# Optimization experiments

Hardware: AMD Instinct MI355X
Metric: run time of the kernel (lower is better)

## Reference

```python
import jax, jax.numpy as jnp
import numpy as np

B, H, W, S = 4, 512, 512, 40
DZ = 0.1            # slice thickness
FOCUS_SLICE = 25    # back-propagation slice count
Z_PLANE = 2.0       # focus plane offset
PAD = 32            # output crop


def setup_inputs() -> dict:
    key = jax.random.key(0)
    ks = jax.random.split(key, 8)
    sample_re = jax.random.normal(ks[0], (B, H, W, S), jnp.float32) * 0.01
    sample_im = jax.random.normal(ks[1], (B, H, W, S), jnp.float32) * 0.01
    planewave_re = jax.random.normal(ks[2], (B, H, W), jnp.float32)
    planewave_im = jax.random.normal(ks[3], (B, H, W), jnp.float32)
    # kz strictly positive so 1/(2*kz) is finite (mask + nan-fix kept for faithfulness)
    kz = jax.random.uniform(ks[4], (H, W), jnp.float32) + 0.5
    otf_abs = jax.random.uniform(ks[5], (H, W), jnp.float32)
    green_mask = (jax.random.uniform(ks[6], (H, W), jnp.float32) < 0.7).astype(jnp.float32)
    otf_phase = jax.random.normal(ks[7], (H, W), jnp.float32) * 0.1
    return dict(sample_re=sample_re, sample_im=sample_im,
                planewave_re=planewave_re, planewave_im=planewave_im,
                kz=kz, otf_abs=otf_abs, green_mask=green_mask, otf_phase=otf_phase)


def reference(sample_re, sample_im, planewave_re, planewave_im, kz, otf_abs, green_mask, otf_phase):
    sample = (sample_re + 1j * sample_im).astype(jnp.complex64)        # [B,H,W,S]
    planewave = (planewave_re + 1j * planewave_im).astype(jnp.complex64)  # [B,H,W]
    kzc = kz.astype(jnp.complex64)

    # module constants: prop_kernel = exp(prop_kernel_pha * dz), prop_kernel_pha = 1j*kz
    prop_kernel = jnp.exp(1j * kzc * DZ)                               # [H,W]
    green = (1j * prop_kernel / (2.0 * kzc)) * green_mask.astype(jnp.complex64)
    green = jnp.where(jnp.isnan(green), jnp.zeros((), green.dtype), green)

    # _propegate_to_last_slice_Multi_Born (oblique_factor=None)
    inc0 = jnp.fft.fft2(planewave)                                     # fft over last two dims
    sample_s = jnp.moveaxis(sample, -1, 0)                             # [S,B,H,W]

    def step(inc, slab):
        u = inc * prop_kernel
        scat = green * jnp.fft.fft2(jnp.fft.ifft2(inc) * slab * DZ)
        return u + scat, None

    inc, _ = jax.lax.scan(step, inc0, sample_s)

    # _propegate_to_center_focus_slice
    pk_center = jnp.conj(prop_kernel ** FOCUS_SLICE)
    pk_focus = prop_kernel ** (Z_PLANE / DZ)
    inc = inc * pk_center * pk_focus

    # _pupil_constrain_abs_square_output with OTF_input provided
    otf_update = (otf_abs * jnp.exp(1j * otf_phase)).astype(jnp.complex64)
    out = jnp.fft.ifft2(inc * otf_update[None])
    return jnp.abs(out)[:, PAD:-PAD, PAD:-PAD]                          # [B, H-2*PAD, W-2*PAD]
```

## Files before the change

### kernel.cpp

```cpp
#include <hip/hip_runtime.h>
#include <math.h>

#define HW_ (512 * 512)

__device__ inline float2 cadd(float2 a, float2 b){ return make_float2(a.x+b.x, a.y+b.y); }
__device__ inline float2 csub(float2 a, float2 b){ return make_float2(a.x-b.x, a.y-b.y); }
__device__ inline float2 cmulf(float2 a, float2 b){ return make_float2(a.x*b.x-a.y*b.y, a.x*b.y+a.y*b.x); }
__device__ inline float bf2f(unsigned short u){ return __uint_as_float(((unsigned int)u) << 16); }
__device__ inline unsigned short f2bf(float f){
    unsigned int x = __float_as_uint(f);
    x += 0x7fffu + ((x >> 16) & 1u);
    return (unsigned short)(x >> 16);
}

template<bool INV>
__device__ inline void dft8(const float2 a[8], float2 X[8]) {
    const float C = 0.70710678118654752440f;
    float2 t0 = cadd(a[0], a[4]), t4 = csub(a[0], a[4]);
    float2 t1 = cadd(a[1], a[5]), d1 = csub(a[1], a[5]);
    float2 t2 = cadd(a[2], a[6]), d2 = csub(a[2], a[6]);
    float2 t3 = cadd(a[3], a[7]), d3 = csub(a[3], a[7]);
    float2 t5, t6, t7;
    if (!INV) {
        t5 = make_float2(C*(d1.x + d1.y), C*(d1.y - d1.x));
        t6 = make_float2(d2.y, -d2.x);
        t7 = make_float2(C*(d3.y - d3.x), -C*(d3.x + d3.y));
    } else {
        t5 = make_float2(C*(d1.x - d1.y), C*(d1.y + d1.x));
        t6 = make_float2(-d2.y, d2.x);
        t7 = make_float2(-C*(d3.x + d3.y), C*(d3.x - d3.y));
    }
    float2 u0 = cadd(t0, t2), u2 = csub(t0, t2);
    float2 u1 = cadd(t1, t3), e3 = csub(t1, t3);
    float2 u3 = INV ? make_float2(-e3.y, e3.x) : make_float2(e3.y, -e3.x);
    float2 u4 = cadd(t4, t6), u6 = csub(t4, t6);
    float2 u5 = cadd(t5, t7), e7 = csub(t5, t7);
    float2 u7 = INV ? make_float2(-e7.y, e7.x) : make_float2(e7.y, -e7.x);
    X[0] = cadd(u0, u1); X[4] = csub(u0, u1);
    X[2] = cadd(u2, u3); X[6] = csub(u2, u3);
    X[1] = cadd(u4, u5); X[5] = csub(u4, u5);
    X[3] = cadd(u6, u7); X[7] = csub(u6, u7);
}

template<bool INV>
__device__ inline void fft512_reg(float2 a[8], float2* __restrict__ xch,
                                  int lane, float2 T1, float2 T2)
{
    float2 tw1 = INV ? make_float2(T1.x, -T1.y) : T1;
    float2 tw2 = INV ? make_float2(T2.x, -T2.y) : T2;
    const int rdo = lane + (lane >> 3);
    float2 b[8];

    dft8<INV>(a, b);
    { float2 w = tw1;
      #pragma unroll
      for (int k = 1; k < 8; ++k) { b[k] = cmulf(b[k], w); w = cmulf(w, tw1); } }
    #pragma unroll
    for (int k = 0; k < 8; ++k) xch[9*lane + k] = b[k];
    __asm__ volatile("s_waitcnt lgkmcnt(0)" ::: "memory");
    #pragma unroll
    for (int j = 0; j < 8; ++j) a[j] = xch[rdo + 72*j];

    dft8<INV>(a, b);
    { float2 w = tw2;
      #pragma unroll
      for (int k = 1; k < 8; ++k) { b[k] = cmulf(b[k], w); w = cmulf(w, tw2); } }
    { const int wbase = (lane & 7) + 72 * (lane >> 3);
      #pragma unroll
      for (int k = 0; k < 8; ++k) xch[wbase + 9*k] = b[k]; }
    __asm__ volatile("s_waitcnt lgkmcnt(0)" ::: "memory");
    #pragma unroll
    for (int j = 0; j < 8; ++j) b[j] = xch[rdo + 72*j];

    dft8<INV>(b, a);
}

__global__ __launch_bounds__(256)
void k_pre(const float* __restrict__ kz, const float* __restrict__ otfa,
           const float* __restrict__ gmask, const float* __restrict__ otfp,
           float2* __restrict__ propT, float2* __restrict__ greenT,
           float2* __restrict__ MT)
{
    __shared__ float2 tp[32*33], tg[32*33], tm[32*33];
    const int tid = threadIdx.x;
    const int w0 = (blockIdx.x & 15) << 5;
    const int h0 = (blockIdx.x >> 4) << 5;
    const int ww = tid & 31, hh = tid >> 5;
    #pragma unroll
    for (int p = 0; p < 4; ++p) {
        int h = hh + p*8;
        int idx = (h0 + h)*512 + w0 + ww;
        float k = kz[idx];
        float sn, cs; __sincosf(k * 0.1f, &sn, &cs);
        float inv2 = 0.5f / k * gmask[idx];
        float phase = otfp[idx] - k * 0.5f;
        float s2, c2; __sincosf(phase, &s2, &c2);
        float oa = otfa[idx];
        tp[h*33 + ww] = make_float2(cs, sn);
        tg[h*33 + ww] = make_float2(-sn*inv2, cs*inv2);
        tm[h*33 + ww] = make_float2(oa*c2, oa*s2);
    }
    __syncthreads();
    #pragma unroll
    for (int p = 0; p < 4; ++p) {
        int wrow = hh + p*8;
        size_t o = (size_t)(w0 + wrow)*512 + h0 + ww;
        propT[o]  = tp[ww*33 + wrow];
        greenT[o] = tg[ww*33 + wrow];
        MT[o]     = tm[ww*33 + wrow];
    }
}

__global__ __launch_bounds__(256)
void k_transpose(const float* __restrict__ sre, const float* __restrict__ sim,
                 ushort2* __restrict__ sampT)
{
    __shared__ ushort2 tile[40 * 129];
    const int bh = blockIdx.x;
    const int b = bh >> 9, h = bh & 511;
    const size_t src_base = (size_t)bh * (512 * 40);
    const float2* sre2 = (const float2*)(sre + src_base);
    const float2* sim2 = (const float2*)(sim + src_base);
    for (int chunk = 0; chunk < 4; ++chunk) {
        const int w0 = chunk * 128;
        const int base2 = w0 * 20;
        __syncthreads();
        for (int j = threadIdx.x; j < 128 * 20; j += 256) {
            float2 re = sre2[base2 + j];
            float2 im = sim2[base2 + j];
            int w = j / 20;
            int s = (j - w * 20) * 2;
            tile[s*129 + w]       = make_ushort2(f2bf(re.x), f2bf(im.x));
            tile[(s+1)*129 + w]   = make_ushort2(f2bf(re.y), f2bf(im.y));
        }
        __syncthreads();
        for (int j = threadIdx.x; j < 40 * 64; j += 256) {
            int s = j >> 6, w2 = (j & 63) << 1;
            ushort2 u0 = tile[s*129 + w2], u1 = tile[s*129 + w2 + 1];
            *(ushort4*)&sampT[(((size_t)s*4 + b)*512 + h)*512 + w0 + w2] =
                make_ushort4(u0.x, u0.y, u1.x, u1.y);
        }
    }
}

__global__ __launch_bounds__(256)
void k_row(float2* __restrict__ fld,
           const float* __restrict__ pwre, const float* __restrict__ pwim,
           const ushort2* __restrict__ sampT,
           float* __restrict__ finout,
           int mode, int slice)
{
    __shared__ float2 xchall[4 * 576];
    const int tid = threadIdx.x, lane = tid & 63, wv = tid >> 6;
    float2* xch = &xchall[wv * 576];
    float s1, c1, s2, c2;
    __sincosf(-6.2831853071795864769f * (float)lane / 512.0f, &s1, &c1);
    __sincosf(-6.2831853071795864769f * (float)(lane >> 3) / 64.0f, &s2, &c2);
    const float2 T1 = make_float2(c1, s1), T2 = make_float2(c2, s2);

    const int r = blockIdx.x * 4 + wv;
    int b, h;
    if (mode == 2) { b = r / 448; h = 32 + (r - b * 448); }
    else           { b = r >> 9;  h = r & 511; }
    const size_t rbase = ((size_t)b * 512 + h) * 512;
    float2 a[8];

    if (mode == 0) {
        #pragma unroll
        for (int j = 0; j < 8; ++j) {
            int w = lane + (j << 6);
            a[j] = make_float2(pwre[rbase + w], pwim[rbase + w]);
        }
        fft512_reg<false>(a, xch, lane, T1, T2);
        #pragma unroll
        for (int j = 0; j < 8; ++j) fld[rbase + lane + (j << 6)] = a[j];
        return;
    }

    #pragma unroll
    for (int j = 0; j < 8; ++j) a[j] = fld[rbase + lane + (j << 6)];
    fft512_reg<true>(a, xch, lane, T1, T2);

    if (mode == 2) {
        float* orow = finout + ((size_t)b * 448 + (h - 32)) * 448;
        #pragma unroll
        for (int j = 0; j < 8; ++j) {
            int w = lane + (j << 6);
            if (w >= 32 && w < 480) {
                float2 v = a[j];
                orow[w - 32] = sqrtf(v.x*v.x + v.y*v.y) * (1.0f / 512.0f);
            }
        }
        return;
    }

    const float scale = 0.1f / 512.0f;
    const size_t sbase = (((size_t)slice * 4 + b) * 512 + h) * 512;
    #pragma unroll
    for (int j = 0; j < 8; ++j) {
        int w = lane + (j << 6);
        ushort2 u = sampT[sbase + w];
        float sr = bf2f(u.x), si = bf2f(u.y);
        float2 v = a[j];
        a[j] = make_float2((v.x*sr - v.y*si) * scale, (v.x*si + v.y*sr) * scale);
    }
    fft512_reg<false>(a, xch, lane, T1, T2);
    #pragma unroll
    for (int j = 0; j < 8; ++j) fld[rbase + lane + (j << 6)] = a[j];
}

__global__ __launch_bounds__(512)
void k_col(float2* __restrict__ fld,
           float2* __restrict__ incT,
           const float2* __restrict__ propT, const float2* __restrict__ greenT,
           const float2* __restrict__ MT, int mode)
{
    __shared__ float2 tile[512 * 9];
    const int tid = threadIdx.x;
    const int lane = tid & 63, wv = tid >> 6;
    const int b = blockIdx.x >> 6;
    const int w0 = (blockIdx.x & 63) << 3;
    const int c = tid & 7, hb = tid >> 3;
    const size_t gbase = (size_t)b * HW_ + w0;

    float s1, c1, s2, c2;
    __sincosf(-6.2831853071795864769f * (float)lane / 512.0f, &s1, &c1);
    __sincosf(-6.2831853071795864769f * (float)(lane >> 3) / 64.0f, &s2, &c2);
    const float2 T1 = make_float2(c1, s1), T2 = make_float2(c2, s2);

    #pragma unroll
    for (int j = 0; j < 8; ++j) {
        int h = hb + (j << 6);
        tile[h*9 + c] = fld[gbase + (size_t)h * 512 + c];
    }
    __syncthreads();
    float2 a[8];
    const int w = w0 + wv;
    #pragma unroll
    for (int j = 0; j < 8; ++j) a[j] = tile[(lane + (j << 6)) * 9 + wv];
    __syncthreads();
    float2* xch = &tile[wv * 576];

    fft512_reg<false>(a, xch, lane, T1, T2);

    const size_t ibase = ((size_t)b * 512 + w) * 512;
    const size_t pbase = (size_t)w * 512;
    if (mode == 0) {
        #pragma unroll
        for (int k = 0; k < 8; ++k) incT[ibase + lane + (k << 6)] = a[k];
        return;
    }
    #pragma unroll
    for (int k = 0; k < 8; ++k) {
        int h = lane + (k << 6);
        float2 p  = propT[pbase + h];
        float2 g  = greenT[pbase + h];
        float2 io = incT[ibase + h];
        float2 nw = make_float2(p.x*io.x - p.y*io.y + g.x*a[k].x - g.y*a[k].y,
                                p.x*io.y + p.y*io.x + g.x*a[k].y + g.y*a[k].x);
        if (mode == 2) nw = cmulf(nw, MT[pbase + h]);
        else           incT[ibase + h] = nw;
        a[k] = nw;
    }

    fft512_reg<true>(a, xch, lane, T1, T2);
    __syncthreads();
    const float inv = 1.0f / 512.0f;
    #pragma unroll
    for (int k = 0; k < 8; ++k)
        tile[(lane + (k << 6)) * 9 + wv] = make_float2(a[k].x * inv, a[k].y * inv);
    __syncthreads();
    #pragma unroll
    for (int j = 0; j < 8; ++j) {
        int h = hb + (j << 6);
        fld[gbase + (size_t)h * 512 + c] = tile[h*9 + c];
    }
}

extern "C" void kernel_launch(void* const* d_in, const int* in_sizes, int n_in,
                              void* d_out, int out_size, void* d_ws, size_t ws_size,
                              hipStream_t stream)
{
    (void)in_sizes; (void)n_in; (void)out_size; (void)ws_size;
    const float* sre   = (const float*)d_in[0];
    const float* simg  = (const float*)d_in[1];
    const float* pwre  = (const float*)d_in[2];
    const float* pwim  = (const float*)d_in[3];
    const float* kz    = (const float*)d_in[4];
    const float* otfa  = (const float*)d_in[5];
    const float* gmask = (const float*)d_in[6];
    const float* otfp  = (const float*)d_in[7];

    char* ws = (char*)d_ws;
    size_t off = 0;
    float2* propT  = (float2*)(ws + off); off += (size_t)HW_ * 8;
    float2* greenT = (float2*)(ws + off); off += (size_t)HW_ * 8;
    float2* MT     = (float2*)(ws + off); off += (size_t)HW_ * 8;
    float2* incT   = (float2*)(ws + off); off += (size_t)4 * HW_ * 8;
    float2* fld    = (float2*)(ws + off); off += (size_t)4 * HW_ * 8;
    ushort2* sampT = (ushort2*)(ws + off);

    k_pre<<<256, 256, 0, stream>>>(kz, otfa, gmask, otfp, propT, greenT, MT);
    k_transpose<<<2048, 256, 0, stream>>>(sre, simg, sampT);

    k_row<<<512, 256, 0, stream>>>(fld, pwre, pwim, nullptr, nullptr, 0, 0);
    k_col<<<256, 512, 0, stream>>>(fld, incT, propT, greenT, MT, 0);

    for (int s = 0; s < 40; ++s) {
        k_row<<<512, 256, 0, stream>>>(fld, nullptr, nullptr, sampT, nullptr, 1, s);
        k_col<<<256, 512, 0, stream>>>(fld, incT, propT, greenT, MT, (s == 39) ? 2 : 1);
    }
    k_row<<<448, 256, 0, stream>>>(fld, nullptr, nullptr, nullptr, (float*)d_out, 2, 0);
}
```

Before: 1.359 ms.

## Drop incT buffer by keeping field row-FFT form and storing scattered field in fp16

Rather than keeping the spectrum incT in a separate transposed buffer, k_col now redoes the column FFT of the row-transformed field fldA each step. The scattered term goes through a new fp16 buffer written by k_row, so incT is never read or written. The transpose kernel is also rebuilt to use four times more blocks, float4 loads and an XOR-swizzled shared tile with 16-byte stores. This cuts global traffic per slice and the 8 MB incT stream, but it adds a second column FFT per step and fp16 rounding error on the scattered field.

```diff
diff --git a/kernel.cpp b/kernel.cpp
--- a/kernel.cpp
+++ b/kernel.cpp
@@ -1,4 +1,5 @@
 #include <hip/hip_runtime.h>
+#include <hip/hip_fp16.h>
 #include <math.h>
 
 #define HW_ (512 * 512)
@@ -115,36 +116,40 @@
 void k_transpose(const float* __restrict__ sre, const float* __restrict__ sim,
                  ushort2* __restrict__ sampT)
 {
-    __shared__ ushort2 tile[40 * 129];
-    const int bh = blockIdx.x;
+    __shared__ __align__(16) ushort2 tile[40 * 128];
+    const int bh = blockIdx.x >> 2;
+    const int chunk = blockIdx.x & 3;
     const int b = bh >> 9, h = bh & 511;
-    const size_t src_base = (size_t)bh * (512 * 40);
-    const float2* sre2 = (const float2*)(sre + src_base);
-    const float2* sim2 = (const float2*)(sim + src_base);
-    for (int chunk = 0; chunk < 4; ++chunk) {
-        const int w0 = chunk * 128;
-        const int base2 = w0 * 20;
-        __syncthreads();
-        for (int j = threadIdx.x; j < 128 * 20; j += 256) {
-            float2 re = sre2[base2 + j];
-            float2 im = sim2[base2 + j];
-            int w = j / 20;
-            int s = (j - w * 20) * 2;
-            tile[s*129 + w]       = make_ushort2(f2bf(re.x), f2bf(im.x));
-            tile[(s+1)*129 + w]   = make_ushort2(f2bf(re.y), f2bf(im.y));
-        }
-        __syncthreads();
-        for (int j = threadIdx.x; j < 40 * 64; j += 256) {
-            int s = j >> 6, w2 = (j & 63) << 1;
-            ushort2 u0 = tile[s*129 + w2], u1 = tile[s*129 + w2 + 1];
-            *(ushort4*)&sampT[(((size_t)s*4 + b)*512 + h)*512 + w0 + w2] =
-                make_ushort4(u0.x, u0.y, u1.x, u1.y);
-        }
+    const int w0 = chunk << 7;
+    const float4* sre4 = (const float4*)(sre + (size_t)bh * 20480) + chunk * 1280;
+    const float4* sim4 = (const float4*)(sim + (size_t)bh * 20480) + chunk * 1280;
+    #pragma unroll
+    for (int i = 0; i < 5; ++i) {
+        int j = threadIdx.x + (i << 8);
+        float4 re = sre4[j];
+        float4 im = sim4[j];
+        int w = j / 10;
+        int m = j - w * 10;
+        ushort2* row = &tile[(m << 2) * 128 + (w ^ ((m & 7) << 2))];
+        row[0]   = make_ushort2(f2bf(re.x), f2bf(im.x));
+        row[128] = make_ushort2(f2bf(re.y), f2bf(im.y));
+        row[256] = make_ushort2(f2bf(re.z), f2bf(im.z));
+        row[384] = make_ushort2(f2bf(re.w), f2bf(im.w));
+    }
+    __syncthreads();
+    #pragma unroll
+    for (int i = 0; i < 5; ++i) {
+        int j = threadIdx.x + (i << 8);
+        int s = j >> 5, q = j & 31;
+        int qp = q ^ ((s >> 2) & 7);
+        uint4 v = *(const uint4*)&tile[(s << 7) + (qp << 2)];
+        *(uint4*)&sampT[(((size_t)s * 4 + b) * 512 + h) * 512 + w0 + (q << 2)] = v;
     }
 }
 
 __global__ __launch_bounds__(256)
-void k_row(float2* __restrict__ fld,
+void k_row(float2* __restrict__ fldA,
+           ushort2* __restrict__ fld2,
            const float* __restrict__ pwre, const float* __restrict__ pwim,
            const ushort2* __restrict__ sampT,
            float* __restrict__ finout,
@@ -173,12 +178,12 @@
         }
         fft512_reg<false>(a, xch, lane, T1, T2);
         #pragma unroll
-        for (int j = 0; j < 8; ++j) fld[rbase + lane + (j << 6)] = a[j];
+        for (int j = 0; j < 8; ++j) fldA[rbase + lane + (j << 6)] = a[j];
         return;
     }
 
     #pragma unroll
-    for (int j = 0; j < 8; ++j) a[j] = fld[rbase + lane + (j << 6)];
+    for (int j = 0; j < 8; ++j) a[j] = fldA[rbase + lane + (j << 6)];
     fft512_reg<true>(a, xch, lane, T1, T2);
 
     if (mode == 2) {
@@ -206,16 +211,22 @@
     }
     fft512_reg<false>(a, xch, lane, T1, T2);
     #pragma unroll
-    for (int j = 0; j < 8; ++j) fld[rbase + lane + (j << 6)] = a[j];
+    for (int j = 0; j < 8; ++j) {
+        float2 v = a[j];
+        fld2[rbase + lane + (j << 6)] =
+            make_ushort2(__half_as_ushort(__float2half(v.x)),
+                         __half_as_ushort(__float2half(v.y)));
+    }
 }
 
 __global__ __launch_bounds__(512)
-void k_col(float2* __restrict__ fld,
-           float2* __restrict__ incT,
+void k_col(float2* __restrict__ fldA,
+           const ushort2* __restrict__ fld2,
            const float2* __restrict__ propT, const float2* __restrict__ greenT,
-           const float2* __restrict__ MT, int mode)
-{
-    __shared__ float2 tile[512 * 9];
+           const float2* __restrict__ MT, int last)
+{
+    __shared__ float2 tileA[512 * 9];
+    __shared__ ushort2 tile2[512 * 9];
     const int tid = threadIdx.x;
     const int lane = tid & 63, wv = tid >> 6;
     const int b = blockIdx.x >> 6;
@@ -231,49 +242,49 @@
     #pragma unroll
     for (int j = 0; j < 8; ++j) {
         int h = hb + (j << 6);
-        tile[h*9 + c] = fld[gbase + (size_t)h * 512 + c];
-    }
-    __syncthreads();
-    float2 a[8];
+        tileA[h*9 + c] = fldA[gbase + (size_t)h * 512 + c];
+        tile2[h*9 + c] = fld2[gbase + (size_t)h * 512 + c];
+    }
+    __syncthreads();
+    float2 aA[8], aS[8];
+    #pragma unroll
+    for (int j = 0; j < 8; ++j) {
+        int idx = (lane + (j << 6)) * 9 + wv;
+        aA[j] = tileA[idx];
+        ushort2 u = tile2[idx];
+        aS[j] = make_float2(__half2float(__ushort_as_half(u.x)),
+                            __half2float(__ushort_as_half(u.y)));
+    }
+    __syncthreads();
+    float2* xch = &tileA[wv * 576];
+
+    fft512_reg<false>(aA, xch, lane, T1, T2);
+    fft512_reg<false>(aS, xch, lane, T1, T2);
+
     const int w = w0 + wv;
-    #pragma unroll
-    for (int j = 0; j < 8; ++j) a[j] = tile[(lane + (j << 6)) * 9 + wv];
-    __syncthreads();
-    float2* xch = &tile[wv * 576];
-
-    fft512_reg<false>(a, xch, lane, T1, T2);
-
-    const size_t ibase = ((size_t)b * 512 + w) * 512;
     const size_t pbase = (size_t)w * 512;
-    if (mode == 0) {
-        #pragma unroll
-        for (int k = 0; k < 8; ++k) incT[ibase + lane + (k << 6)] = a[k];
-        return;
-    }
     #pragma unroll
     for (int k = 0; k < 8; ++k) {
         int h = lane + (k << 6);
         float2 p  = propT[pbase + h];
         float2 g  = greenT[pbase + h];
-        float2 io = incT[ibase + h];
-        float2 nw = make_float2(p.x*io.x - p.y*io.y + g.x*a[k].x - g.y*a[k].y,
-                                p.x*io.y + p.y*io.x + g.x*a[k].y + g.y*a[k].x);
-        if (mode == 2) nw = cmulf(nw, MT[pbase + h]);
-        else           incT[ibase + h] = nw;
-        a[k] = nw;
-    }
-
-    fft512_reg<true>(a, xch, lane, T1, T2);
+        float2 nw = make_float2(p.x*aA[k].x - p.y*aA[k].y + g.x*aS[k].x - g.y*aS[k].y,
+                                p.x*aA[k].y + p.y*aA[k].x + g.x*aS[k].y + g.y*aS[k].x);
+        if (last) nw = cmulf(nw, MT[pbase + h]);
+        aA[k] = nw;
+    }
+
+    fft512_reg<true>(aA, xch, lane, T1, T2);
     __syncthreads();
     const float inv = 1.0f / 512.0f;
     #pragma unroll
     for (int k = 0; k < 8; ++k)
-        tile[(lane + (k << 6)) * 9 + wv] = make_float2(a[k].x * inv, a[k].y * inv);
+        tileA[(lane + (k << 6)) * 9 + wv] = make_float2(aA[k].x * inv, aA[k].y * inv);
     __syncthreads();
     #pragma unroll
     for (int j = 0; j < 8; ++j) {
         int h = hb + (j << 6);
-        fld[gbase + (size_t)h * 512 + c] = tile[h*9 + c];
+        fldA[gbase + (size_t)h * 512 + c] = tileA[h*9 + c];
     }
 }
 
@@ -296,19 +307,18 @@
     float2* propT  = (float2*)(ws + off); off += (size_t)HW_ * 8;
     float2* greenT = (float2*)(ws + off); off += (size_t)HW_ * 8;
     float2* MT     = (float2*)(ws + off); off += (size_t)HW_ * 8;
-    float2* incT   = (float2*)(ws + off); off += (size_t)4 * HW_ * 8;
-    float2* fld    = (float2*)(ws + off); off += (size_t)4 * HW_ * 8;
+    float2* fldA   = (float2*)(ws + off); off += (size_t)4 * HW_ * 8;
+    ushort2* fld2  = (ushort2*)(ws + off); off += (size_t)4 * HW_ * 4;
     ushort2* sampT = (ushort2*)(ws + off);
 
     k_pre<<<256, 256, 0, stream>>>(kz, otfa, gmask, otfp, propT, greenT, MT);
-    k_transpose<<<2048, 256, 0, stream>>>(sre, simg, sampT);
-
-    k_row<<<512, 256, 0, stream>>>(fld, pwre, pwim, nullptr, nullptr, 0, 0);
-    k_col<<<256, 512, 0, stream>>>(fld, incT, propT, greenT, MT, 0);
+    k_transpose<<<8192, 256, 0, stream>>>(sre, simg, sampT);
+
+    k_row<<<512, 256, 0, stream>>>(fldA, nullptr, pwre, pwim, nullptr, nullptr, 0, 0);
 
     for (int s = 0; s < 40; ++s) {
-        k_row<<<512, 256, 0, stream>>>(fld, nullptr, nullptr, sampT, nullptr, 1, s);
-        k_col<<<256, 512, 0, stream>>>(fld, incT, propT, greenT, MT, (s == 39) ? 2 : 1);
-    }
-    k_row<<<448, 256, 0, stream>>>(fld, nullptr, nullptr, nullptr, (float*)d_out, 2, 0);
-}
+        k_row<<<512, 256, 0, stream>>>(fldA, fld2, nullptr, nullptr, sampT, nullptr, 1, s);
+        k_col<<<256, 512, 0, stream>>>(fldA, fld2, propT, greenT, MT, (s == 39) ? 1 : 0);
+    }
+    k_row<<<448, 256, 0, stream>>>(fldA, nullptr, nullptr, nullptr, nullptr, (float*)d_out, 2, 0);
+}
```

New measurement: 1.259 ms. 7.4% less time.
